# Performance work log

Measured on AMD Instinct MI355X. Metric: run time of the kernel, lower is better.

Reference implementation:

```python
import jax, jax.numpy as jnp
import numpy as np

C, G, S, L, B = 16, 8192, 8, 3, 32


def setup_inputs() -> dict:
    key = jax.random.key(0)
    kx, kI = jax.random.split(key)
    # x: valuation vector over G ground atoms per batch element, in [0,1)
    x = jax.random.uniform(kx, (B, G), dtype=jnp.float32)
    # I: precomputed index tensor [C, G, S, L], indices into the G axis of x
    I = jax.random.randint(kI, (C, G, S, L), 0, G, dtype=jnp.int64)
    return {"x": x, "I": I}


def reference(x, I):
    # Equivalent of: for each clause i, gather(V_tild, 1, I_i) -> prod over L -> sum over S
    # torch gather semantics: out[b, g, s, l] = x[b, I[i, g, s, l]]
    # Vectorized over all clauses at once; no repeat/broadcast materialization beyond the gather.
    gathered = x[:, I]                        # [B, C, G, S, L]
    body = jnp.prod(gathered, axis=-1)        # conjunction over L body literals -> [B, C, G, S]
    clause_val = jnp.sum(body, axis=-1)       # sum over S substitutions -> [B, C, G]
    # torch.stack over clauses puts C first: [C, B, G]
    return jnp.transpose(clause_val, (1, 0, 2))
```

## Files before the change

### kernel.cpp

```cpp
#include <hip/hip_runtime.h>
#include <hip/hip_fp16.h>
#include <stdint.h>

#define Cc 16
#define Gg 8192
#define Ss 8
#define Ll 3
#define Bb 32

#define BH 4
#define NZ (Bb / BH)
#define THREADS 512
#define ITERS 2
#define GCH (THREADS * ITERS)
#define NGC (Gg / GCH)

__device__ __forceinline__ void clause_eval(const uint2* __restrict__ xl2,
                                            const int4 q[6], float acc[4]) {
    #pragma unroll
    for (int h = 0; h < 2; ++h) {
        const int4 qa = q[3 * h + 0];
        const int4 qb = q[3 * h + 1];
        const int4 qc = q[3 * h + 2];
        int idx[12] = {qa.x, qa.y, qa.z, qa.w,
                       qb.x, qb.y, qb.z, qb.w,
                       qc.x, qc.y, qc.z, qc.w};
        uint2 r[12];
        #pragma unroll
        for (int k = 0; k < 12; ++k)
            r[k] = xl2[(uint32_t)idx[k]];
        #pragma unroll
        for (int s = 0; s < 4; ++s) {
            const uint2 ra = r[3 * s + 0];
            const uint2 rb = r[3 * s + 1];
            const uint2 rd = r[3 * s + 2];
            __half2 p0 = __hmul2(__hmul2(*(const __half2*)&ra.x,
                                         *(const __half2*)&rb.x),
                                 *(const __half2*)&rd.x);
            __half2 p1 = __hmul2(__hmul2(*(const __half2*)&ra.y,
                                         *(const __half2*)&rb.y),
                                 *(const __half2*)&rd.y);
            float2 f0 = __half22float2(p0);
            float2 f1 = __half22float2(p1);
            acc[0] += f0.x;
            acc[1] += f0.y;
            acc[2] += f1.x;
            acc[3] += f1.y;
        }
    }
}

__global__ __launch_bounds__(THREADS, 4) void clause_f16_p2(
        const float* __restrict__ x, const int* __restrict__ I,
        float* __restrict__ out) {
    __shared__ uint2 xl[Gg];
    const int tid = threadIdx.x;

    const int lb = (blockIdx.x & 7) * (1024 / 8) + (blockIdx.x >> 3);
    const int zh = lb & (NZ - 1);
    const int gc = (lb >> 3) & (NGC - 1);
    const int c  = lb >> 6;
    const int gbase = gc * GCH;

    const int g0 = gbase + tid;
    const int g1 = gbase + THREADS + tid;
    const int4* ip0 = (const int4*)(I + ((size_t)c * Gg + g0) * (Ss * Ll));
    const int4* ip1 = (const int4*)(I + ((size_t)c * Gg + g1) * (Ss * Ll));
    int4 q0[6], q1[6];
    #pragma unroll
    for (int k = 0; k < 6; ++k) q0[k] = ip0[k];
    #pragma unroll
    for (int k = 0; k < 6; ++k) q1[k] = ip1[k];

    {
        const float* xs = x + (size_t)(BH * zh) * Gg;
        #pragma unroll 4
        for (int k = 0; k < Gg / (2 * THREADS); ++k) {
            const int g = 2 * (tid + k * THREADS);
            float2 v0 = *(const float2*)&xs[g];
            float2 v1 = *(const float2*)&xs[Gg + g];
            float2 v2 = *(const float2*)&xs[2 * (size_t)Gg + g];
            float2 v3 = *(const float2*)&xs[3 * (size_t)Gg + g];
            __half2 a01 = __floats2half2_rn(v0.x, v1.x);
            __half2 a23 = __floats2half2_rn(v2.x, v3.x);
            __half2 b01 = __floats2half2_rn(v0.y, v1.y);
            __half2 b23 = __floats2half2_rn(v2.y, v3.y);
            uint4 w = make_uint4(*(const uint32_t*)&a01, *(const uint32_t*)&a23,
                                 *(const uint32_t*)&b01, *(const uint32_t*)&b23);
            *(uint4*)&xl[g] = w;
        }
    }

    __syncthreads();

    float* opb = out + ((size_t)(c * Bb + BH * zh)) * Gg;

    {
        float acc[4] = {0, 0, 0, 0};
        clause_eval(xl, q0, acc);
        #pragma unroll
        for (int j = 0; j < 4; ++j)
            opb[(size_t)j * Gg + g0] = acc[j];
    }
    {
        float acc[4] = {0, 0, 0, 0};
        clause_eval(xl, q1, acc);
        #pragma unroll
        for (int j = 0; j < 4; ++j)
            opb[(size_t)j * Gg + g1] = acc[j];
    }
}

extern "C" void kernel_launch(void* const* d_in, const int* in_sizes, int n_in,
                              void* d_out, int out_size, void* d_ws, size_t ws_size,
                              hipStream_t stream) {
    const float* x = (const float*)d_in[0];
    const int* I = (const int*)d_in[1];
    float* out = (float*)d_out;
    (void)d_ws; (void)ws_size;

    const int grid = Cc * NGC * NZ;
    clause_f16_p2<<<grid, THREADS, 0, stream>>>(x, I, out);
}
```

Measured before the change: 81.01 us.

## Process two clauses per block to amortize shared-memory x staging

Each block now handles two clauses for the same batch slice and G chunk, which halves the grid to 512 blocks and halves how often the fp16 x table is rebuilt in LDS. The x staging uses float4 loads that are all issued before conversion. Index loads for the next clause/chunk are software-pipelined behind evaluation of the current one. Outputs are written with nontemporal stores. The trade-off is fewer blocks for latency hiding and more register pressure from the double-buffered index arrays.

Result: no change. 80.55 us (-0.6%).

```diff
diff --git a/kernel.cpp b/kernel.cpp
--- a/kernel.cpp
+++ b/kernel.cpp
@@ -11,9 +11,6 @@
 #define BH 4
 #define NZ (Bb / BH)
 #define THREADS 512
-#define ITERS 2
-#define GCH (THREADS * ITERS)
-#define NGC (Gg / GCH)
 
 __device__ __forceinline__ void clause_eval(const uint2* __restrict__ xl2,
                                             const int4 q[6], float acc[4]) {
@@ -50,64 +47,92 @@
     }
 }
 
-__global__ __launch_bounds__(THREADS, 4) void clause_f16_p2(
+#define EVAL_STORE(QBUF, CVAL, GVAL)                                          \
+    {                                                                         \
+        float acc[4] = {0.f, 0.f, 0.f, 0.f};                                  \
+        clause_eval(xl, QBUF, acc);                                           \
+        float* op = out + ((size_t)((CVAL) * Bb + BH * zh)) * Gg + (GVAL);    \
+        __builtin_nontemporal_store(acc[0], &op[0]);                          \
+        __builtin_nontemporal_store(acc[1], &op[(size_t)Gg]);                 \
+        __builtin_nontemporal_store(acc[2], &op[2 * (size_t)Gg]);             \
+        __builtin_nontemporal_store(acc[3], &op[3 * (size_t)Gg]);             \
+    }
+
+__global__ __launch_bounds__(THREADS, 4) void clause_f16_1r(
         const float* __restrict__ x, const int* __restrict__ I,
         float* __restrict__ out) {
     __shared__ uint2 xl[Gg];
     const int tid = threadIdx.x;
 
-    const int lb = (blockIdx.x & 7) * (1024 / 8) + (blockIdx.x >> 3);
+    const int lb = (blockIdx.x & 7) * 64 + (blockIdx.x >> 3);
     const int zh = lb & (NZ - 1);
-    const int gc = (lb >> 3) & (NGC - 1);
-    const int c  = lb >> 6;
-    const int gbase = gc * GCH;
-
+    const int combo = lb >> 3;
+    const int gc = combo & 7;
+    const int cp = combo >> 3;
+    const int gbase = gc * 1024;
+    const int c0 = 2 * cp, c1 = 2 * cp + 1;
     const int g0 = gbase + tid;
     const int g1 = gbase + THREADS + tid;
-    const int4* ip0 = (const int4*)(I + ((size_t)c * Gg + g0) * (Ss * Ll));
-    const int4* ip1 = (const int4*)(I + ((size_t)c * Gg + g1) * (Ss * Ll));
-    int4 q0[6], q1[6];
+
+    const float* xs = x + (size_t)(BH * zh) * Gg;
+    float4 v[4][4];
     #pragma unroll
-    for (int k = 0; k < 6; ++k) q0[k] = ip0[k];
+    for (int k = 0; k < 4; ++k) {
+        const int g = 4 * tid + k * (4 * THREADS);
+        #pragma unroll
+        for (int r = 0; r < 4; ++r)
+            v[k][r] = *(const float4*)&xs[(size_t)r * Gg + g];
+    }
+
+    int4 qA[6], qB[6];
+    {
+        const int4* ip = (const int4*)(I + ((size_t)c0 * Gg + g0) * (Ss * Ll));
+        #pragma unroll
+        for (int k = 0; k < 6; ++k) qA[k] = ip[k];
+    }
+
     #pragma unroll
-    for (int k = 0; k < 6; ++k) q1[k] = ip1[k];
-
-    {
-        const float* xs = x + (size_t)(BH * zh) * Gg;
-        #pragma unroll 4
-        for (int k = 0; k < Gg / (2 * THREADS); ++k) {
-            const int g = 2 * (tid + k * THREADS);
-            float2 v0 = *(const float2*)&xs[g];
-            float2 v1 = *(const float2*)&xs[Gg + g];
-            float2 v2 = *(const float2*)&xs[2 * (size_t)Gg + g];
-            float2 v3 = *(const float2*)&xs[3 * (size_t)Gg + g];
-            __half2 a01 = __floats2half2_rn(v0.x, v1.x);
-            __half2 a23 = __floats2half2_rn(v2.x, v3.x);
-            __half2 b01 = __floats2half2_rn(v0.y, v1.y);
-            __half2 b23 = __floats2half2_rn(v2.y, v3.y);
-            uint4 w = make_uint4(*(const uint32_t*)&a01, *(const uint32_t*)&a23,
-                                 *(const uint32_t*)&b01, *(const uint32_t*)&b23);
-            *(uint4*)&xl[g] = w;
-        }
+    for (int k = 0; k < 4; ++k) {
+        const int g = 4 * tid + k * (4 * THREADS);
+        const float4 r0 = v[k][0], r1 = v[k][1], r2 = v[k][2], r3 = v[k][3];
+        __half2 l0 = __floats2half2_rn(r0.x, r1.x);
+        __half2 h0 = __floats2half2_rn(r2.x, r3.x);
+        __half2 l1 = __floats2half2_rn(r0.y, r1.y);
+        __half2 h1 = __floats2half2_rn(r2.y, r3.y);
+        __half2 l2 = __floats2half2_rn(r0.z, r1.z);
+        __half2 h2v = __floats2half2_rn(r2.z, r3.z);
+        __half2 l3 = __floats2half2_rn(r0.w, r1.w);
+        __half2 h3 = __floats2half2_rn(r2.w, r3.w);
+        uint4 w0 = make_uint4(*(const uint32_t*)&l0, *(const uint32_t*)&h0,
+                              *(const uint32_t*)&l1, *(const uint32_t*)&h1);
+        uint4 w1 = make_uint4(*(const uint32_t*)&l2, *(const uint32_t*)&h2v,
+                              *(const uint32_t*)&l3, *(const uint32_t*)&h3);
+        *(uint4*)&xl[g] = w0;
+        *(uint4*)&xl[g + 2] = w1;
     }
 
     __syncthreads();
 
-    float* opb = out + ((size_t)(c * Bb + BH * zh)) * Gg;
-
     {
-        float acc[4] = {0, 0, 0, 0};
-        clause_eval(xl, q0, acc);
+        const int4* ip = (const int4*)(I + ((size_t)c0 * Gg + g1) * (Ss * Ll));
         #pragma unroll
-        for (int j = 0; j < 4; ++j)
-            opb[(size_t)j * Gg + g0] = acc[j];
+        for (int k = 0; k < 6; ++k) qB[k] = ip[k];
+        EVAL_STORE(qA, c0, g0)
     }
     {
-        float acc[4] = {0, 0, 0, 0};
-        clause_eval(xl, q1, acc);
+        const int4* ip = (const int4*)(I + ((size_t)c1 * Gg + g0) * (Ss * Ll));
         #pragma unroll
-        for (int j = 0; j < 4; ++j)
-            opb[(size_t)j * Gg + g1] = acc[j];
+        for (int k = 0; k < 6; ++k) qA[k] = ip[k];
+        EVAL_STORE(qB, c0, g1)
+    }
+    {
+        const int4* ip = (const int4*)(I + ((size_t)c1 * Gg + g1) * (Ss * Ll));
+        #pragma unroll
+        for (int k = 0; k < 6; ++k) qB[k] = ip[k];
+        EVAL_STORE(qA, c1, g0)
+    }
+    {
+        EVAL_STORE(qB, c1, g1)
     }
 }
 
@@ -119,6 +144,6 @@
     float* out = (float*)d_out;
     (void)d_ws; (void)ws_size;
 
-    const int grid = Cc * NGC * NZ;
-    clause_f16_p2<<<grid, THREADS, 0, stream>>>(x, I, out);
+    const int grid = 512;
+    clause_f16_1r<<<grid, THREADS, 0, stream>>>(x, I, out);
 }
```
